# Kernel tuning notes

Hardware: AMD Instinct MI355X
Metric: run time of the kernel (lower is better)

## Reference

```python
import jax, jax.numpy as jnp
import numpy as np

N = 100000
E = 1600000
IN = 128
HID = 32
HEADS = 4
HID2 = 8  # hidden_channels / 4
OUT = 1


def setup_inputs() -> dict:
    key = jax.random.key(0)
    ks = jax.random.split(key, 13)
    def glorot(k, shape):
        fan = sum(shape[-2:]) if len(shape) >= 2 else shape[-1]
        return jax.random.normal(k, shape, dtype=jnp.float32) * (2.0 / fan) ** 0.5
    return {
        "x": jax.random.normal(ks[0], (N, IN), dtype=jnp.float32),
        "edge_index": jax.random.randint(ks[1], (2, E), 0, N, dtype=jnp.int32),
        "edge_attr": jax.random.normal(ks[2], (E, 8), dtype=jnp.float32),  # ignored by GATConv (edge_dim=None)
        "W1": glorot(ks[3], (IN, HEADS * HID)),
        "a_src1": glorot(ks[4], (HEADS, HID)),
        "a_dst1": glorot(ks[5], (HEADS, HID)),
        "b1": jnp.zeros((HEADS * HID,), dtype=jnp.float32),
        "W2": glorot(ks[6], (HEADS * HID, 1 * HID2)),
        "a_src2": glorot(ks[7], (1, HID2)),
        "a_dst2": glorot(ks[8], (1, HID2)),
        "b2": jnp.zeros((HID2,), dtype=jnp.float32),
        "Wlin": glorot(ks[9], (HID2, OUT)),
        "blin": jnp.zeros((OUT,), dtype=jnp.float32),
    }


def gat_layer(x, W, a_src, a_dst, bias, src, dst, num_nodes, concat):
    """PyG GATConv (edge_dim=None): gather -> LeakyReLU attn -> segment softmax over dst -> scatter-add."""
    H, C = a_src.shape
    h = (x @ W).reshape(num_nodes, H, C)                        # [N, H, C]
    alpha_s = jnp.einsum('nhc,hc->nh', h, a_src)                # [N, H]
    alpha_d = jnp.einsum('nhc,hc->nh', h, a_dst)
    e = jax.nn.leaky_relu(alpha_s[src] + alpha_d[dst], 0.2)     # [E, H]
    m = jax.ops.segment_max(e, dst, num_segments=num_nodes)     # softmax over incoming edges per dst
    ex = jnp.exp(e - m[dst])
    denom = jax.ops.segment_sum(ex, dst, num_segments=num_nodes)
    alpha = ex / (denom[dst] + 1e-16)                           # [E, H]
    out = jax.ops.segment_sum(h[src] * alpha[:, :, None], dst, num_segments=num_nodes)  # [N, H, C]
    out = out.reshape(num_nodes, H * C) if concat else out.mean(axis=1)
    return out + bias


def reference(x, edge_index, edge_attr, W1, a_src1, a_dst1, b1, W2, a_src2, a_dst2, b2, Wlin, blin):
    n = x.shape[0]
    loops = jnp.arange(n, dtype=edge_index.dtype)               # add_self_loops=True (PyG default)
    src = jnp.concatenate([edge_index[0], loops])
    dst = jnp.concatenate([edge_index[1], loops])
    h = jax.nn.elu(gat_layer(x, W1, a_src1, a_dst1, b1, src, dst, n, True))
    h = jax.nn.elu(gat_layer(h, W2, a_src2, a_dst2, b2, src, dst, n, False))
    return jax.nn.sigmoid(h @ Wlin + blin)                      # [N, 1]
```

## Files before the change

### kernel.cpp

```cpp
#include <hip/hip_runtime.h>
#include <hip/hip_bf16.h>

__device__ __forceinline__ float lrelu02(float v) { return v > 0.f ? v : 0.2f * v; }

__device__ __forceinline__ float bf2f(unsigned short u) {
    union { unsigned int i; float f; } v; v.i = ((unsigned int)u) << 16; return v.f;
}
__device__ __forceinline__ unsigned short f2bf(float f) {
    union { float f; unsigned int i; } v; v.f = f;
    unsigned int x = v.i;
    return (unsigned short)((x + 0x7fffu + ((x >> 16) & 1u)) >> 16);
}
__device__ __forceinline__ float blo(unsigned int u) {
    union { unsigned int i; float f; } v; v.i = u << 16; return v.f;
}
__device__ __forceinline__ float bhi(unsigned int u) {
    union { unsigned int i; float f; } v; v.i = u & 0xffff0000u; return v.f;
}

typedef float f32x4 __attribute__((ext_vector_type(4)));
typedef short s16x8 __attribute__((ext_vector_type(8)));

__global__ __launch_bounds__(512) void gemm1_k(
    const float* __restrict__ x, const float* __restrict__ W1,
    const float* __restrict__ aw_s, const float* __restrict__ aw_d,
    unsigned short* __restrict__ h1b, float* __restrict__ as1, float* __restrict__ ad1, int N,
    const int* __restrict__ ei, int E, int* __restrict__ deg, int* __restrict__ rank)
{
    {
        const int total = E + N;
        const int stride = gridDim.x * 512;
        for (int e = blockIdx.x * 512 + threadIdx.x; e < total; e += stride) {
            int d = (e < E) ? ei[E + e] : (e - E);
            rank[e] = atomicAdd(&deg[d], 1);
        }
    }

    __shared__ unsigned short Wt[128 * 128];
    {
        const float4* W4 = (const float4*)W1;
        for (int i = threadIdx.x; i < 128 * 32; i += 512) {
            float4 f = W4[i];
            int k = i >> 5, c4 = (i & 31) * 4;
            #pragma unroll
            for (int j = 0; j < 4; ++j) {
                int col = c4 + j;
                float fv = j == 0 ? f.x : j == 1 ? f.y : j == 2 ? f.z : f.w;
                Wt[col * 128 + (k ^ ((col & 7) << 3))] = f2bf(fv);
            }
        }
    }

    const int lane = threadIdx.x & 63;
    const int wv   = threadIdx.x >> 6;
    const int li   = lane & 15;
    const int kg   = lane >> 2 >> 2;
    const int row0 = blockIdx.x * 128 + wv * 16;

    const int rc = (row0 + li < N) ? (row0 + li) : (N - 1);
    const float4* xr = (const float4*)(x + (size_t)rc * 128);

    f32x4 acc[8];
    #pragma unroll
    for (int ct = 0; ct < 8; ++ct) acc[ct] = {0.f, 0.f, 0.f, 0.f};

    __syncthreads();

    #pragma unroll
    for (int ks = 0; ks < 4; ++ks) {
        float4 f0 = xr[ks * 8 + kg * 2];
        float4 f1 = xr[ks * 8 + kg * 2 + 1];
        float xf[8] = {f0.x, f0.y, f0.z, f0.w, f1.x, f1.y, f1.z, f1.w};
        s16x8 ahi, alo;
        #pragma unroll
        for (int j = 0; j < 8; ++j) {
            unsigned short h = f2bf(xf[j]);
            ahi[j] = (short)h;
            alo[j] = (short)f2bf(xf[j] - bf2f(h));
        }
        const int kbase = ks * 32 + kg * 8;
        #pragma unroll
        for (int ct = 0; ct < 8; ++ct) {
            const int col = ct * 16 + li;
            const s16x8 b = *reinterpret_cast<const s16x8*>(
                Wt + col * 128 + (kbase ^ ((col & 7) << 3)));
            acc[ct] = __builtin_amdgcn_mfma_f32_16x16x32_bf16(ahi, b, acc[ct], 0, 0, 0);
            acc[ct] = __builtin_amdgcn_mfma_f32_16x16x32_bf16(alo, b, acc[ct], 0, 0, 0);
        }
    }

    float aws_[8], awd_[8];
    #pragma unroll
    for (int t = 0; t < 8; ++t) { aws_[t] = aw_s[t * 16 + li]; awd_[t] = aw_d[t * 16 + li]; }

    #pragma unroll
    for (int i = 0; i < 4; ++i) {
        const int gr = row0 + (lane >> 4) * 4 + i;
        const bool valid = gr < N;
        float s0 = acc[0][i] * aws_[0] + acc[1][i] * aws_[1];
        float s1 = acc[2][i] * aws_[2] + acc[3][i] * aws_[3];
        float s2 = acc[4][i] * aws_[4] + acc[5][i] * aws_[5];
        float s3 = acc[6][i] * aws_[6] + acc[7][i] * aws_[7];
        float d0 = acc[0][i] * awd_[0] + acc[1][i] * awd_[1];
        float d1 = acc[2][i] * awd_[2] + acc[3][i] * awd_[3];
        float d2 = acc[4][i] * awd_[4] + acc[5][i] * awd_[5];
        float d3 = acc[6][i] * awd_[6] + acc[7][i] * awd_[7];
        #pragma unroll
        for (int m = 1; m < 16; m <<= 1) {
            s0 += __shfl_xor(s0, m, 16); s1 += __shfl_xor(s1, m, 16);
            s2 += __shfl_xor(s2, m, 16); s3 += __shfl_xor(s3, m, 16);
            d0 += __shfl_xor(d0, m, 16); d1 += __shfl_xor(d1, m, 16);
            d2 += __shfl_xor(d2, m, 16); d3 += __shfl_xor(d3, m, 16);
        }
        if (valid) {
            if (li < 4) {
                float sv = li == 0 ? s0 : li == 1 ? s1 : li == 2 ? s2 : s3;
                float dv = li == 0 ? d0 : li == 1 ? d1 : li == 2 ? d2 : d3;
                as1[gr * 4 + li] = sv;
                ad1[gr * 4 + li] = dv;
            }
            #pragma unroll
            for (int ct = 0; ct < 8; ++ct)
                h1b[(size_t)gr * 128 + ct * 16 + li] = f2bf(acc[ct][i]);
        }
    }
}

__global__ __launch_bounds__(256) void blocksum_k(
    const int* __restrict__ deg, int N, int* __restrict__ bsum)
{
    __shared__ int sh[256];
    int i = blockIdx.x * 256 + threadIdx.x;
    sh[threadIdx.x] = (i < N) ? deg[i] : 0;
    __syncthreads();
    for (int off = 128; off; off >>= 1) {
        if (threadIdx.x < off) sh[threadIdx.x] += sh[threadIdx.x + off];
        __syncthreads();
    }
    if (threadIdx.x == 0) bsum[blockIdx.x] = sh[0];
}

__global__ __launch_bounds__(1024) void scanbsum_k(int* __restrict__ bsum, int nb)
{
    __shared__ int buf[1024];
    __shared__ int carry;
    if (threadIdx.x == 0) carry = 0;
    __syncthreads();
    for (int base = 0; base < nb; base += 1024) {
        int i = base + threadIdx.x;
        int v = (i < nb) ? bsum[i] : 0;
        buf[threadIdx.x] = v;
        __syncthreads();
        for (int off = 1; off < 1024; off <<= 1) {
            int t = (threadIdx.x >= off) ? buf[threadIdx.x - off] : 0;
            __syncthreads();
            buf[threadIdx.x] += t;
            __syncthreads();
        }
        if (i < nb) bsum[i] = buf[threadIdx.x] - v + carry;
        __syncthreads();
        if (threadIdx.x == 0) carry += buf[1023];
        __syncthreads();
    }
}

__global__ __launch_bounds__(256) void rowptr_k(
    const int* __restrict__ deg, const int* __restrict__ bsum, int N, int E,
    int* __restrict__ rowptr)
{
    __shared__ int buf[256];
    int i = blockIdx.x * 256 + threadIdx.x;
    int v = (i < N) ? deg[i] : 0;
    buf[threadIdx.x] = v;
    __syncthreads();
    for (int off = 1; off < 256; off <<= 1) {
        int t = (threadIdx.x >= off) ? buf[threadIdx.x - off] : 0;
        __syncthreads();
        buf[threadIdx.x] += t;
        __syncthreads();
    }
    if (i < N) rowptr[i] = bsum[blockIdx.x] + buf[threadIdx.x] - v;
    if (i == 0) rowptr[N] = E + N;
}

__global__ __launch_bounds__(256) void place_k(
    const int* __restrict__ ei, int E, int N,
    const int* __restrict__ rank, const int* __restrict__ rowptr,
    int* __restrict__ csr)
{
    int e = blockIdx.x * 256 + threadIdx.x;
    if (e >= E + N) return;
    int s, d;
    if (e < E) { s = ei[e]; d = ei[E + e]; } else { s = d = e - E; }
    csr[rowptr[d] + rank[e]] = s;
}

__global__ __launch_bounds__(256) void gat1_k(
    const int* __restrict__ csr, const int* __restrict__ rowptr,
    const float* __restrict__ as1, const float* __restrict__ ad1,
    const unsigned short* __restrict__ h1b, const float* __restrict__ b1,
    const float* __restrict__ W2, const float* __restrict__ aw_s2, const float* __restrict__ aw_d2,
    float* __restrict__ g, float* __restrict__ as2, float* __restrict__ ad2, int N)
{
    __shared__ float red[4][8][12];
    const int wv   = threadIdx.x >> 6;
    const int wid  = (blockIdx.x * 256 + threadIdx.x) >> 6;
    const int lane = threadIdx.x & 63;
    if (wid >= N) return;
    const int start = rowptr[wid], end = rowptr[wid + 1];
    const int i16 = lane & 15;
    const int hh  = lane >> 4;
    const float adh = ad1[wid * 4 + hh];
    const float mh  = lrelu02(as1[wid * 4 + hh] + adh);
    const unsigned short* hb = h1b + lane * 2;

    float den = 0.f, acc0 = 0.f, acc1 = 0.f;
    int k0 = start;
    for (; k0 + 16 <= end; k0 += 16) {
        int s = csr[k0 + i16];
        float w = __expf(lrelu02(as1[s * 4 + hh] + adh) - mh);
        den += w;
        #pragma unroll
        for (int e = 0; e < 16; ++e) {
            int se = __builtin_amdgcn_readlane(s, e);
            float we = __shfl(w, e, 16);
            unsigned int pv = *(const unsigned int*)(hb + (size_t)se * 128);
            acc0 = fmaf(bf2f((unsigned short)pv), we, acc0);
            acc1 = fmaf(bf2f((unsigned short)(pv >> 16)), we, acc1);
        }
    }
    int cnt = end - k0;
    if (cnt > 0) {
        int s = (i16 < cnt) ? csr[k0 + i16] : wid;
        float w = (i16 < cnt) ? __expf(lrelu02(as1[s * 4 + hh] + adh) - mh) : 0.f;
        den += w;
        for (int e = 0; e < cnt; ++e) {
            int se = __builtin_amdgcn_readlane(s, e);
            float we = __shfl(w, e, 16);
            unsigned int pv = *(const unsigned int*)(hb + (size_t)se * 128);
            acc0 = fmaf(bf2f((unsigned short)pv), we, acc0);
            acc1 = fmaf(bf2f((unsigned short)(pv >> 16)), we, acc1);
        }
    }
    den += __shfl_xor(den, 1); den += __shfl_xor(den, 2);
    den += __shfl_xor(den, 4); den += __shfl_xor(den, 8);
    const float rden = 1.f / (den + 1e-16f);
    float v0 = acc0 * rden + b1[lane * 2];
    float v1 = acc1 * rden + b1[lane * 2 + 1];
    v0 = v0 > 0.f ? v0 : expm1f(v0);
    v1 = v1 > 0.f ? v1 : expm1f(v1);

    const float4 a0 = *(const float4*)(W2 + 16 * lane);
    const float4 a1 = *(const float4*)(W2 + 16 * lane + 4);
    const float4 b0 = *(const float4*)(W2 + 16 * lane + 8);
    const float4 b1v = *(const float4*)(W2 + 16 * lane + 12);
    float p[8];
    p[0] = v0 * a0.x + v1 * b0.x;  p[1] = v0 * a0.y + v1 * b0.y;
    p[2] = v0 * a0.z + v1 * b0.z;  p[3] = v0 * a0.w + v1 * b0.w;
    p[4] = v0 * a1.x + v1 * b1v.x; p[5] = v0 * a1.y + v1 * b1v.y;
    p[6] = v0 * a1.z + v1 * b1v.z; p[7] = v0 * a1.w + v1 * b1v.w;
    #pragma unroll
    for (int j = 0; j < 8; ++j) {
        p[j] += __shfl_xor(p[j], 8);
        p[j] += __shfl_xor(p[j], 16);
        p[j] += __shfl_xor(p[j], 32);
    }
    if (lane < 8) {
        #pragma unroll
        for (int j = 0; j < 8; ++j) red[wv][lane][j] = p[j];
    }
    if (lane < 8) {
        float gj = 0.f;
        #pragma unroll
        for (int c = 0; c < 8; ++c) gj += red[wv][c][lane];
        g[(size_t)wid * 8 + lane] = gj;
        float ts = gj * aw_s2[lane], td = gj * aw_d2[lane];
        ts += __shfl_xor(ts, 1); ts += __shfl_xor(ts, 2); ts += __shfl_xor(ts, 4);
        td += __shfl_xor(td, 1); td += __shfl_xor(td, 2); td += __shfl_xor(td, 4);
        if (lane == 0) { as2[wid] = ts; ad2[wid] = td; }
    }
}

__global__ __launch_bounds__(256) void gat2_k(
    const int* __restrict__ csr, const int* __restrict__ rowptr,
    const float* __restrict__ as2, const float* __restrict__ ad2,
    const float* __restrict__ g, const float* __restrict__ b2_,
    const float* __restrict__ Wlin, const float* __restrict__ blin,
    float* __restrict__ out, int N)
{
    const int wid  = (blockIdx.x * 256 + threadIdx.x) >> 6;
    const int lane = threadIdx.x & 63;
    if (wid >= N) return;
    const int start = rowptr[wid], end = rowptr[wid + 1];
    const int i8  = lane & 7;
    const int grp = lane >> 3;
    const float adh = ad2[wid];
    const float mh  = lrelu02(as2[wid] + adh);
    float den = 0.f, acc = 0.f;
    int k0 = start;
    for (; k0 + 8 <= end; k0 += 8) {
        int s = csr[k0 + i8];
        float w = __expf(lrelu02(as2[s] + adh) - mh);
        den += w;
        int   se = __shfl(s, grp, 8);
        float we = __shfl(w, grp, 8);
        acc = fmaf(we, g[(size_t)se * 8 + i8], acc);
    }
    int cnt = end - k0;
    if (cnt > 0) {
        int s = (i8 < cnt) ? csr[k0 + i8] : wid;
        float w = (i8 < cnt) ? __expf(lrelu02(as2[s] + adh) - mh) : 0.f;
        den += w;
        int   se = __shfl(s, grp, 8);
        float we = __shfl(w, grp, 8);
        acc = fmaf(we, g[(size_t)se * 8 + i8], acc);
    }
    den += __shfl_xor(den, 1); den += __shfl_xor(den, 2); den += __shfl_xor(den, 4);
    acc += __shfl_xor(acc, 8); acc += __shfl_xor(acc, 16); acc += __shfl_xor(acc, 32);
    float v = acc / (den + 1e-16f) + b2_[i8];
    v = v > 0.f ? v : expm1f(v);
    float t = v * Wlin[i8];
    t += __shfl_xor(t, 1); t += __shfl_xor(t, 2); t += __shfl_xor(t, 4);
    if (lane == 0) out[wid] = 1.f / (1.f + __expf(-(t + blin[0])));
}

extern "C" void kernel_launch(void* const* d_in, const int* in_sizes, int n_in,
                              void* d_out, int out_size, void* d_ws, size_t ws_size,
                              hipStream_t stream)
{
    (void)n_in; (void)out_size; (void)ws_size;
    const float* x    = (const float*)d_in[0];
    const int*   ei   = (const int*)d_in[1];
    const float* W1   = (const float*)d_in[3];
    const float* as1w = (const float*)d_in[4];
    const float* ad1w = (const float*)d_in[5];
    const float* b1   = (const float*)d_in[6];
    const float* W2   = (const float*)d_in[7];
    const float* as2w = (const float*)d_in[8];
    const float* ad2w = (const float*)d_in[9];
    const float* b2v  = (const float*)d_in[10];
    const float* Wlin = (const float*)d_in[11];
    const float* blin = (const float*)d_in[12];

    const int N = in_sizes[0] / 128;
    const int E = in_sizes[1] / 2;
    const int total = E + N;

    float* p = (float*)d_ws;
    unsigned short* h1b = (unsigned short*)p; p += (size_t)N * 64;
    float* as1  = p; p += (size_t)N * 4;
    float* ad1  = p; p += (size_t)N * 4;
    float* g    = p; p += (size_t)N * 8;
    float* as2  = p; p += (size_t)N;
    float* ad2  = p; p += (size_t)N;
    int* deg    = (int*)p; p += (size_t)N;
    int* rowptr = (int*)p; p += (size_t)N + 1;
    int* bsum   = (int*)p; p += ((size_t)N + 255) / 256;
    int* rank   = (int*)p; p += (size_t)total;
    int* csr    = (int*)p; p += (size_t)total;

    const int eb = (total + 255) / 256;
    const int nb = (N + 255) / 256;

    hipMemsetAsync(deg, 0, (size_t)N * sizeof(int), stream);
    gemm1_k<<<(N + 127) / 128, 512, 0, stream>>>(x, W1, as1w, ad1w, h1b, as1, ad1, N,
                                                 ei, E, deg, rank);
    blocksum_k<<<nb, 256, 0, stream>>>(deg, N, bsum);
    scanbsum_k<<<1, 1024, 0, stream>>>(bsum, nb);
    rowptr_k<<<nb, 256, 0, stream>>>(deg, bsum, N, E, rowptr);
    place_k<<<eb, 256, 0, stream>>>(ei, E, N, rank, rowptr, csr);

    gat1_k<<<(N * 64 + 255) / 256, 256, 0, stream>>>(csr, rowptr, as1, ad1, h1b, b1,
                                                     W2, as2w, ad2w, g, as2, ad2, N);
    gat2_k<<<(N * 64 + 255) / 256, 256, 0, stream>>>(csr, rowptr, as2, ad2, g, b2v, Wlin, blin,
                                                     (float*)d_out, N);
}
```

Measured before the change: 427.6 us.

## Process four edges per wave in gat1 with lane groups over edges

Restructures the layer-1 aggregation so each 16-lane group handles a different edge, and each lane covers all four heads for two channels, instead of serializing edges via readlane/shfl broadcast. Attention logits are loaded as float4 per source, and the partial sums are reduced across the groups with xor-shuffles at the end. This removes the per-edge broadcast and shuffle loop and the shared-memory reduction, so the wave issues fewer gathers back-to-back. In exchange it adds cross-group shuffles at the end, wastes lanes on the padded tail edges when a node's degree is not a multiple of four, and makes each lane read four scattered 4-byte words per edge instead of one. A cosmetic simplification of kg in gemm1 is also included.

```diff
diff --git a/kernel.cpp b/kernel.cpp
--- a/kernel.cpp
+++ b/kernel.cpp
@@ -54,7 +54,7 @@
     const int lane = threadIdx.x & 63;
     const int wv   = threadIdx.x >> 6;
     const int li   = lane & 15;
-    const int kg   = lane >> 2 >> 2;
+    const int kg   = lane >> 4;
     const int row0 = blockIdx.x * 128 + wv * 16;
 
     const int rc = (row0 + li < N) ? (row0 + li) : (N - 1);
@@ -202,82 +202,109 @@
     const float* __restrict__ W2, const float* __restrict__ aw_s2, const float* __restrict__ aw_d2,
     float* __restrict__ g, float* __restrict__ as2, float* __restrict__ ad2, int N)
 {
-    __shared__ float red[4][8][12];
-    const int wv   = threadIdx.x >> 6;
     const int wid  = (blockIdx.x * 256 + threadIdx.x) >> 6;
     const int lane = threadIdx.x & 63;
     if (wid >= N) return;
     const int start = rowptr[wid], end = rowptr[wid + 1];
-    const int i16 = lane & 15;
-    const int hh  = lane >> 4;
-    const float adh = ad1[wid * 4 + hh];
-    const float mh  = lrelu02(as1[wid * 4 + hh] + adh);
-    const unsigned short* hb = h1b + lane * 2;
-
-    float den = 0.f, acc0 = 0.f, acc1 = 0.f;
-    int k0 = start;
-    for (; k0 + 16 <= end; k0 += 16) {
-        int s = csr[k0 + i16];
-        float w = __expf(lrelu02(as1[s * 4 + hh] + adh) - mh);
-        den += w;
+    const int grp = lane >> 4;
+    const int t   = lane & 15;
+
+    const float4 ad4 = *(const float4*)(ad1 + (size_t)wid * 4);
+    const float4 at4 = *(const float4*)(as1 + (size_t)wid * 4);
+    const float mh0 = lrelu02(at4.x + ad4.x);
+    const float mh1 = lrelu02(at4.y + ad4.y);
+    const float mh2 = lrelu02(at4.z + ad4.z);
+    const float mh3 = lrelu02(at4.w + ad4.w);
+
+    float den0 = 0.f, den1 = 0.f, den2 = 0.f, den3 = 0.f;
+    float acc[4][2];
+    #pragma unroll
+    for (int i = 0; i < 4; ++i) { acc[i][0] = 0.f; acc[i][1] = 0.f; }
+
+    for (int k = start; k < end; k += 4) {
+        const int idx = k + grp;
+        const bool valid = idx < end;
+        const int s = valid ? csr[idx] : wid;
+        const float4 a4 = *(const float4*)(as1 + (size_t)s * 4);
+        float w0 = valid ? __expf(lrelu02(a4.x + ad4.x) - mh0) : 0.f;
+        float w1 = valid ? __expf(lrelu02(a4.y + ad4.y) - mh1) : 0.f;
+        float w2 = valid ? __expf(lrelu02(a4.z + ad4.z) - mh2) : 0.f;
+        float w3 = valid ? __expf(lrelu02(a4.w + ad4.w) - mh3) : 0.f;
+        den0 += w0; den1 += w1; den2 += w2; den3 += w3;
+        const unsigned short* hr = h1b + (size_t)s * 128 + t * 2;
         #pragma unroll
-        for (int e = 0; e < 16; ++e) {
-            int se = __builtin_amdgcn_readlane(s, e);
-            float we = __shfl(w, e, 16);
-            unsigned int pv = *(const unsigned int*)(hb + (size_t)se * 128);
-            acc0 = fmaf(bf2f((unsigned short)pv), we, acc0);
-            acc1 = fmaf(bf2f((unsigned short)(pv >> 16)), we, acc1);
-        }
-    }
-    int cnt = end - k0;
-    if (cnt > 0) {
-        int s = (i16 < cnt) ? csr[k0 + i16] : wid;
-        float w = (i16 < cnt) ? __expf(lrelu02(as1[s * 4 + hh] + adh) - mh) : 0.f;
-        den += w;
-        for (int e = 0; e < cnt; ++e) {
-            int se = __builtin_amdgcn_readlane(s, e);
-            float we = __shfl(w, e, 16);
-            unsigned int pv = *(const unsigned int*)(hb + (size_t)se * 128);
-            acc0 = fmaf(bf2f((unsigned short)pv), we, acc0);
-            acc1 = fmaf(bf2f((unsigned short)(pv >> 16)), we, acc1);
-        }
-    }
-    den += __shfl_xor(den, 1); den += __shfl_xor(den, 2);
-    den += __shfl_xor(den, 4); den += __shfl_xor(den, 8);
-    const float rden = 1.f / (den + 1e-16f);
-    float v0 = acc0 * rden + b1[lane * 2];
-    float v1 = acc1 * rden + b1[lane * 2 + 1];
-    v0 = v0 > 0.f ? v0 : expm1f(v0);
-    v1 = v1 > 0.f ? v1 : expm1f(v1);
-
-    const float4 a0 = *(const float4*)(W2 + 16 * lane);
-    const float4 a1 = *(const float4*)(W2 + 16 * lane + 4);
-    const float4 b0 = *(const float4*)(W2 + 16 * lane + 8);
-    const float4 b1v = *(const float4*)(W2 + 16 * lane + 12);
-    float p[8];
-    p[0] = v0 * a0.x + v1 * b0.x;  p[1] = v0 * a0.y + v1 * b0.y;
-    p[2] = v0 * a0.z + v1 * b0.z;  p[3] = v0 * a0.w + v1 * b0.w;
-    p[4] = v0 * a1.x + v1 * b1v.x; p[5] = v0 * a1.y + v1 * b1v.y;
-    p[6] = v0 * a1.z + v1 * b1v.z; p[7] = v0 * a1.w + v1 * b1v.w;
-    #pragma unroll
-    for (int j = 0; j < 8; ++j) {
-        p[j] += __shfl_xor(p[j], 8);
-        p[j] += __shfl_xor(p[j], 16);
-        p[j] += __shfl_xor(p[j], 32);
-    }
-    if (lane < 8) {
-        #pragma unroll
-        for (int j = 0; j < 8; ++j) red[wv][lane][j] = p[j];
-    }
-    if (lane < 8) {
-        float gj = 0.f;
-        #pragma unroll
-        for (int c = 0; c < 8; ++c) gj += red[wv][c][lane];
-        g[(size_t)wid * 8 + lane] = gj;
-        float ts = gj * aw_s2[lane], td = gj * aw_d2[lane];
-        ts += __shfl_xor(ts, 1); ts += __shfl_xor(ts, 2); ts += __shfl_xor(ts, 4);
-        td += __shfl_xor(td, 1); td += __shfl_xor(td, 2); td += __shfl_xor(td, 4);
-        if (lane == 0) { as2[wid] = ts; ad2[wid] = td; }
+        for (int i = 0; i < 4; ++i) {
+            const unsigned int pv = *(const unsigned int*)(hr + i * 32);
+            const float wi = i == 0 ? w0 : i == 1 ? w1 : i == 2 ? w2 : w3;
+            acc[i][0] = fmaf(wi, blo(pv), acc[i][0]);
+            acc[i][1] = fmaf(wi, bhi(pv), acc[i][1]);
+        }
+    }
+
+    den0 += __shfl_xor(den0, 16); den0 += __shfl_xor(den0, 32);
+    den1 += __shfl_xor(den1, 16); den1 += __shfl_xor(den1, 32);
+    den2 += __shfl_xor(den2, 16); den2 += __shfl_xor(den2, 32);
+    den3 += __shfl_xor(den3, 16); den3 += __shfl_xor(den3, 32);
+    #pragma unroll
+    for (int i = 0; i < 4; ++i) {
+        acc[i][0] += __shfl_xor(acc[i][0], 16); acc[i][0] += __shfl_xor(acc[i][0], 32);
+        acc[i][1] += __shfl_xor(acc[i][1], 16); acc[i][1] += __shfl_xor(acc[i][1], 32);
+    }
+
+    const float rd0 = 1.f / (den0 + 1e-16f);
+    const float rd1 = 1.f / (den1 + 1e-16f);
+    const float rd2 = 1.f / (den2 + 1e-16f);
+    const float rd3 = 1.f / (den3 + 1e-16f);
+
+    float v[4][2];
+    #pragma unroll
+    for (int i = 0; i < 4; ++i) {
+        const int c = i * 32 + t * 2;
+        const float rdi = i == 0 ? rd0 : i == 1 ? rd1 : i == 2 ? rd2 : rd3;
+        float v0 = acc[i][0] * rdi + b1[c];
+        float v1 = acc[i][1] * rdi + b1[c + 1];
+        v[i][0] = v0 > 0.f ? v0 : expm1f(v0);
+        v[i][1] = v1 > 0.f ? v1 : expm1f(v1);
+    }
+
+    float p0 = 0.f, p1 = 0.f, p2 = 0.f, p3 = 0.f, p4 = 0.f, p5 = 0.f, p6 = 0.f, p7 = 0.f;
+    #pragma unroll
+    for (int i = 0; i < 4; ++i) {
+        const int c = i * 32 + t * 2;
+        const float4 wa = *(const float4*)(W2 + c * 8);
+        const float4 wb = *(const float4*)(W2 + c * 8 + 4);
+        const float4 wc = *(const float4*)(W2 + c * 8 + 8);
+        const float4 wd = *(const float4*)(W2 + c * 8 + 12);
+        p0 += v[i][0] * wa.x + v[i][1] * wc.x;
+        p1 += v[i][0] * wa.y + v[i][1] * wc.y;
+        p2 += v[i][0] * wa.z + v[i][1] * wc.z;
+        p3 += v[i][0] * wa.w + v[i][1] * wc.w;
+        p4 += v[i][0] * wb.x + v[i][1] * wd.x;
+        p5 += v[i][0] * wb.y + v[i][1] * wd.y;
+        p6 += v[i][0] * wb.z + v[i][1] * wd.z;
+        p7 += v[i][0] * wb.w + v[i][1] * wd.w;
+    }
+    #pragma unroll
+    for (int m = 1; m < 16; m <<= 1) {
+        p0 += __shfl_xor(p0, m, 16); p1 += __shfl_xor(p1, m, 16);
+        p2 += __shfl_xor(p2, m, 16); p3 += __shfl_xor(p3, m, 16);
+        p4 += __shfl_xor(p4, m, 16); p5 += __shfl_xor(p5, m, 16);
+        p6 += __shfl_xor(p6, m, 16); p7 += __shfl_xor(p7, m, 16);
+    }
+
+    if (lane == 0) {
+        float4 g0 = {p0, p1, p2, p3};
+        float4 g1 = {p4, p5, p6, p7};
+        *(float4*)(g + (size_t)wid * 8)     = g0;
+        *(float4*)(g + (size_t)wid * 8 + 4) = g1;
+        const float4 s0 = *(const float4*)(aw_s2);
+        const float4 s1 = *(const float4*)(aw_s2 + 4);
+        const float4 d0 = *(const float4*)(aw_d2);
+        const float4 d1 = *(const float4*)(aw_d2 + 4);
+        as2[wid] = p0 * s0.x + p1 * s0.y + p2 * s0.z + p3 * s0.w
+                 + p4 * s1.x + p5 * s1.y + p6 * s1.z + p7 * s1.w;
+        ad2[wid] = p0 * d0.x + p1 * d0.y + p2 * d0.z + p3 * d0.w
+                 + p4 * d1.x + p5 * d1.y + p6 * d1.z + p7 * d1.w;
     }
 }
 
```

Measured after the change: 498.9 us. 16.7% more time.
